# Kernel tuning notes

Hardware: AMD Instinct MI355X
Metric: run time of the kernel (lower is better)

The kernel has to match this reference:

```python
import jax, jax.numpy as jnp
import numpy as np

B, NX, NY = 16, 1024, 1024
DIN_X, DIN_Y = 768, 283
DK, DV, NH = 80, 80, 8
HK, HV = DK // NH, DV // NH  # 10, 10
NORM = 1.0 / np.sqrt(HK)


def setup_inputs() -> dict:
    key = jax.random.key(0)
    kx, ky, kq, kk, kv = jax.random.split(key, 5)
    x = jax.random.normal(kx, (B, NX, DIN_X), dtype=jnp.float32)
    y = jax.random.normal(ky, (B, NY, DIN_Y), dtype=jnp.float32)
    attn_mask = jnp.zeros((B, NX, NY), dtype=jnp.float32)  # unused in forward (dead arg in original)
    # torch nn.Linear weights are [out, in]; kaiming-uniform-ish init scale
    Wq = jax.random.normal(kq, (DK, DIN_X), dtype=jnp.float32) / np.sqrt(DIN_X)
    Wk = jax.random.normal(kk, (DK, DIN_Y), dtype=jnp.float32) / np.sqrt(DIN_Y)
    Wv = jax.random.normal(kv, (DV, DIN_Y), dtype=jnp.float32) / np.sqrt(DIN_Y)
    return {"x": x, "y": y, "attn_mask": attn_mask, "Wq": Wq, "Wk": Wk, "Wv": Wv}


def reference(x, y, attn_mask, Wq, Wk, Wv):
    b, n_x, _ = x.shape
    n_y = y.shape[1]
    # projections (Linear, no bias): [B,N,D] @ W^T
    q = (x @ Wq.T).reshape(b, n_x, NH, HK).transpose(0, 2, 1, 3)  # [B,H,Nx,hk]
    k = (y @ Wk.T).reshape(b, n_y, NH, HK).transpose(0, 2, 1, 3)  # [B,H,Ny,hk]
    v = (y @ Wv.T).reshape(b, n_y, NH, HV).transpose(0, 2, 1, 3)  # [B,H,Ny,hv]
    scores = jnp.einsum("bhqd,bhkd->bhqk", q, k) * NORM          # [B,H,Nx,Ny]
    dist = jax.nn.softmax(scores, axis=-1)
    # dropout p=0.5 is identity in eval mode
    att = jnp.einsum("bhqk,bhkd->bhqd", dist, v)                  # [B,H,Nx,hv]
    att = att.transpose(0, 2, 1, 3).reshape(b, n_x, DV)           # [B,Nx,dim_v]
    return att, dist
```

## Files before the change

### kernel.cpp

```cpp
#include <hip/hip_runtime.h>
#include <hip/hip_bf16.h>

#define BB 16
#define NXX 1024
#define NYY 1024
#define DINX 768
#define DINY 283
#define NHH 8
#define HKK 10
#define DKV 80
#define NORMF 0.31622776601683794f

#define QT 32
#define KC 128
#define SLD 1040

__global__ __launch_bounds__(256) void proj_q_kernel(
    const float* __restrict__ X, const float* __restrict__ W, float* __restrict__ Out) {
  const int LDP = 68;
  __shared__ float Xs[32 * 68];
  __shared__ float Ws[80 * 68];
  const int t = threadIdx.x;
  const int rb = blockIdx.x * 32;
  const int tc = t & 15;
  const int tr = t >> 4;

  float acc[2][5];
#pragma unroll
  for (int i = 0; i < 2; ++i)
#pragma unroll
    for (int j = 0; j < 5; ++j) acc[i][j] = 0.f;

  for (int ch = 0; ch < 12; ++ch) {
    const int dk = ch << 6;
    __syncthreads();
#pragma unroll
    for (int i = 0; i < 8; ++i) {
      int idx = i * 256 + t;
      int r = idx >> 6, c = idx & 63;
      Xs[r * LDP + c] = X[(size_t)(rb + r) * DINX + dk + c];
    }
#pragma unroll
    for (int i = 0; i < 20; ++i) {
      int idx = i * 256 + t;
      int r = idx >> 6, c = idx & 63;
      Ws[r * LDP + c] = W[(size_t)r * DINX + dk + c];
    }
    __syncthreads();
#pragma unroll
    for (int dv = 0; dv < 16; ++dv) {
      float4 xv[2], wv[5];
#pragma unroll
      for (int i = 0; i < 2; ++i)
        xv[i] = *(const float4*)&Xs[(tr * 2 + i) * LDP + dv * 4];
#pragma unroll
      for (int j = 0; j < 5; ++j)
        wv[j] = *(const float4*)&Ws[(tc + 16 * j) * LDP + dv * 4];
#pragma unroll
      for (int i = 0; i < 2; ++i)
#pragma unroll
        for (int j = 0; j < 5; ++j) {
          acc[i][j] += xv[i].x * wv[j].x;
          acc[i][j] += xv[i].y * wv[j].y;
          acc[i][j] += xv[i].z * wv[j].z;
          acc[i][j] += xv[i].w * wv[j].w;
        }
    }
  }
#pragma unroll
  for (int i = 0; i < 2; ++i)
#pragma unroll
    for (int j = 0; j < 5; ++j)
      Out[(size_t)(rb + tr * 2 + i) * DKV + tc + 16 * j] = acc[i][j];
}

__global__ __launch_bounds__(256) void proj_kv_kernel(
    const float* __restrict__ Y, const float* __restrict__ WK, const float* __restrict__ WV,
    float* __restrict__ OutK, float* __restrict__ OutV) {
  const int LDP = 36;
  __shared__ float Xs[32 * 36];
  __shared__ float Ws[160 * 36];
  const int t = threadIdx.x;
  const int rb = blockIdx.x * 32;
  const int tc = t & 15;
  const int tr = t >> 4;

  float acc[2][10];
#pragma unroll
  for (int i = 0; i < 2; ++i)
#pragma unroll
    for (int j = 0; j < 10; ++j) acc[i][j] = 0.f;

  for (int ch = 0; ch < 9; ++ch) {
    const int dk = ch << 5;
    __syncthreads();
#pragma unroll
    for (int i = 0; i < 4; ++i) {
      int idx = i * 256 + t;
      int r = idx >> 5, c = idx & 31;
      int d = dk + c;
      Xs[r * LDP + c] = (d < DINY) ? Y[(size_t)(rb + r) * DINY + d] : 0.f;
    }
#pragma unroll
    for (int i = 0; i < 20; ++i) {
      int idx = i * 256 + t;
      int r = idx >> 5, c = idx & 31;
      int d = dk + c;
      float v = 0.f;
      if (d < DINY) v = (r < 80) ? WK[(size_t)r * DINY + d] : WV[(size_t)(r - 80) * DINY + d];
      Ws[r * LDP + c] = v;
    }
    __syncthreads();
#pragma unroll
    for (int dv = 0; dv < 8; ++dv) {
      float4 xv[2], wv[10];
#pragma unroll
      for (int i = 0; i < 2; ++i)
        xv[i] = *(const float4*)&Xs[(tr * 2 + i) * LDP + dv * 4];
#pragma unroll
      for (int j = 0; j < 5; ++j) {
        wv[j] = *(const float4*)&Ws[(tc + 16 * j) * LDP + dv * 4];
        wv[5 + j] = *(const float4*)&Ws[(80 + tc + 16 * j) * LDP + dv * 4];
      }
#pragma unroll
      for (int i = 0; i < 2; ++i)
#pragma unroll
        for (int j = 0; j < 10; ++j) {
          acc[i][j] += xv[i].x * wv[j].x;
          acc[i][j] += xv[i].y * wv[j].y;
          acc[i][j] += xv[i].z * wv[j].z;
          acc[i][j] += xv[i].w * wv[j].w;
        }
    }
  }
#pragma unroll
  for (int i = 0; i < 2; ++i)
#pragma unroll
    for (int j = 0; j < 5; ++j) {
      OutK[(size_t)(rb + tr * 2 + i) * DKV + tc + 16 * j] = acc[i][j];
      OutV[(size_t)(rb + tr * 2 + i) * DKV + tc + 16 * j] = acc[i][5 + j];
    }
}

__global__ __launch_bounds__(512) void attn_kernel(
    const float* __restrict__ Qw, const float* __restrict__ Kw,
    const float* __restrict__ Vw, float* __restrict__ out_att,
    float* __restrict__ out_dist) {
  __shared__ __hip_bfloat16 S[QT * SLD];
  __shared__ float Ks[KC * 12];
  __shared__ float Vs[KC * 12];
  __shared__ float rls[QT];

  const int t = threadIdx.x;
  const int bid = blockIdx.x;
  const int qt = bid & 31;
  const int h = (bid >> 5) & 7;
  const int b = bid >> 8;

  const int q = t >> 4;
  const int kl = t & 15;
  const int qg = qt * QT + q;

  float qr[10];
  {
    const float2* qp = (const float2*)(Qw + ((size_t)b * NXX + qg) * DKV + h * HKK);
#pragma unroll
    for (int dd = 0; dd < 5; ++dd) {
      float2 v = qp[dd];
      qr[2 * dd] = v.x * NORMF;
      qr[2 * dd + 1] = v.y * NORMF;
    }
  }

  float acc[10];
#pragma unroll
  for (int d = 0; d < 10; ++d) acc[d] = 0.f;
  float lsum = 0.f;

  for (int ch = 0; ch < NYY / KC; ++ch) {
    __syncthreads();
    if (t < 2 * KC) {
      const int r = t & (KC - 1);
      const float2* src = (const float2*)(((t < KC) ? Kw : Vw) +
          ((size_t)b * NYY + ch * KC + r) * DKV + h * HKK);
      float2* dst = (float2*)(((t < KC) ? Ks : Vs) + r * 12);
#pragma unroll
      for (int dd = 0; dd < 5; ++dd) dst[dd] = src[dd];
    }
    __syncthreads();
#pragma unroll
    for (int j = 0; j < KC / 16; ++j) {
      const int k = (j << 4) + kl;
      const float* kp = &Ks[k * 12];
      float4 k0 = *(const float4*)kp;
      float4 k1 = *(const float4*)(kp + 4);
      float2 k2 = *(const float2*)(kp + 8);
      float s = qr[0] * k0.x + qr[1] * k0.y + qr[2] * k0.z + qr[3] * k0.w +
                qr[4] * k1.x + qr[5] * k1.y + qr[6] * k1.z + qr[7] * k1.w +
                qr[8] * k2.x + qr[9] * k2.y;
      float p = __expf(s);
      lsum += p;
      const float* vp = &Vs[k * 12];
      float4 v0 = *(const float4*)vp;
      float4 v1 = *(const float4*)(vp + 4);
      float2 v2 = *(const float2*)(vp + 8);
      acc[0] += p * v0.x; acc[1] += p * v0.y; acc[2] += p * v0.z; acc[3] += p * v0.w;
      acc[4] += p * v1.x; acc[5] += p * v1.y; acc[6] += p * v1.z; acc[7] += p * v1.w;
      acc[8] += p * v2.x; acc[9] += p * v2.y;
      S[q * SLD + (ch << 7) + k] = __float2bfloat16(p);
    }
  }

#pragma unroll
  for (int o = 8; o; o >>= 1) {
    lsum += __shfl_xor(lsum, o);
#pragma unroll
    for (int d = 0; d < 10; ++d) acc[d] += __shfl_xor(acc[d], o);
  }
  const float rl = 1.0f / lsum;

  if (kl == 0) {
    rls[q] = rl;
    float2* ap = (float2*)(out_att + ((size_t)b * NXX + qg) * DKV + h * HKK);
#pragma unroll
    for (int dd = 0; dd < 5; ++dd)
      ap[dd] = make_float2(acc[2 * dd] * rl, acc[2 * dd + 1] * rl);
  }
  __syncthreads();

  const size_t dbase = (((size_t)(b * NHH + h)) * NXX + qt * QT) * NYY;
#pragma unroll 2
  for (int it = 0; it < 16; ++it) {
    const int e = it * 2048 + t * 4;
    const int qq = e >> 10;
    const int kk = e & 1023;
    uint2 w = *(const uint2*)&S[qq * SLD + kk];
    const float rlq = rls[qq];
    float4 o;
    o.x = __uint_as_float(w.x << 16) * rlq;
    o.y = __uint_as_float(w.x & 0xffff0000u) * rlq;
    o.z = __uint_as_float(w.y << 16) * rlq;
    o.w = __uint_as_float(w.y & 0xffff0000u) * rlq;
    *(float4*)(out_dist + dbase + (size_t)qq * NYY + kk) = o;
  }
}

extern "C" void kernel_launch(void* const* d_in, const int* in_sizes, int n_in,
                              void* d_out, int out_size, void* d_ws, size_t ws_size,
                              hipStream_t stream) {
  (void)in_sizes; (void)n_in; (void)out_size; (void)ws_size;
  const float* x = (const float*)d_in[0];
  const float* y = (const float*)d_in[1];
  const float* Wq = (const float*)d_in[3];
  const float* Wk = (const float*)d_in[4];
  const float* Wv = (const float*)d_in[5];

  float* out = (float*)d_out;
  float* att_out = out;
  float* dist_out = out + (size_t)BB * NXX * DKV;

  float* Qw = (float*)d_ws;
  float* Kw = Qw + (size_t)BB * NXX * DKV;
  float* Vw = Kw + (size_t)BB * NYY * DKV;

  proj_q_kernel<<<NXX * BB / 32, 256, 0, stream>>>(x, Wq, Qw);
  proj_kv_kernel<<<NYY * BB / 32, 256, 0, stream>>>(y, Wk, Wv, Kw, Vw);
  attn_kernel<<<BB * NHH * 32, 512, 0, stream>>>(Qw, Kw, Vw, att_out, dist_out);
}
```

Measured before the change: 463.0 us.

## Register-block four queries per thread in attention and merge projection kernels

After: 1.574 ms. +240.0%, slower.

```diff
diff --git a/kernel.cpp b/kernel.cpp
--- a/kernel.cpp
+++ b/kernel.cpp
@@ -15,134 +15,108 @@
 #define KC 128
 #define SLD 1040
 
-__global__ __launch_bounds__(256) void proj_q_kernel(
-    const float* __restrict__ X, const float* __restrict__ W, float* __restrict__ Out) {
-  const int LDP = 68;
-  __shared__ float Xs[32 * 68];
-  __shared__ float Ws[80 * 68];
+__global__ __launch_bounds__(512, 4) void proj_kernel(
+    const float* __restrict__ X, const float* __restrict__ Y,
+    const float* __restrict__ Wq, const float* __restrict__ Wk, const float* __restrict__ Wv,
+    float* __restrict__ Qw, float* __restrict__ Kw, float* __restrict__ Vw) {
+  __shared__ float Xs[64 * 68];
+  __shared__ float Ws[160 * 68];
   const int t = threadIdx.x;
-  const int rb = blockIdx.x * 32;
+  const bool isQ = (blockIdx.x < 256);
+  const int rb = (isQ ? blockIdx.x : blockIdx.x - 256) * 64;
   const int tc = t & 15;
   const int tr = t >> 4;
 
-  float acc[2][5];
-#pragma unroll
-  for (int i = 0; i < 2; ++i)
-#pragma unroll
-    for (int j = 0; j < 5; ++j) acc[i][j] = 0.f;
-
-  for (int ch = 0; ch < 12; ++ch) {
-    const int dk = ch << 6;
-    __syncthreads();
-#pragma unroll
-    for (int i = 0; i < 8; ++i) {
-      int idx = i * 256 + t;
-      int r = idx >> 6, c = idx & 63;
-      Xs[r * LDP + c] = X[(size_t)(rb + r) * DINX + dk + c];
-    }
-#pragma unroll
-    for (int i = 0; i < 20; ++i) {
-      int idx = i * 256 + t;
-      int r = idx >> 6, c = idx & 63;
-      Ws[r * LDP + c] = W[(size_t)r * DINX + dk + c];
-    }
-    __syncthreads();
-#pragma unroll
-    for (int dv = 0; dv < 16; ++dv) {
-      float4 xv[2], wv[5];
-#pragma unroll
-      for (int i = 0; i < 2; ++i)
-        xv[i] = *(const float4*)&Xs[(tr * 2 + i) * LDP + dv * 4];
+  if (isQ) {
+    float acc[2][5];
+#pragma unroll
+    for (int i = 0; i < 2; ++i)
+#pragma unroll
+      for (int j = 0; j < 5; ++j) acc[i][j] = 0.f;
+
+    for (int ch = 0; ch < 12; ++ch) {
+      const int dk = ch << 6;
+      __syncthreads();
+      for (int u = t; u < 1024; u += 512) {
+        int r = u >> 4, c4 = u & 15;
+        *(float4*)&Xs[r * 68 + c4 * 4] = *(const float4*)&X[(size_t)(rb + r) * DINX + dk + c4 * 4];
+      }
+      for (int u = t; u < 1280; u += 512) {
+        int r = u >> 4, c4 = u & 15;
+        *(float4*)&Ws[r * 68 + c4 * 4] = *(const float4*)&Wq[(size_t)r * DINX + dk + c4 * 4];
+      }
+      __syncthreads();
+#pragma unroll
+      for (int dv = 0; dv < 16; ++dv) {
+        float4 xv0 = *(const float4*)&Xs[(tr * 2 + 0) * 68 + dv * 4];
+        float4 xv1 = *(const float4*)&Xs[(tr * 2 + 1) * 68 + dv * 4];
+        float4 wv[5];
+#pragma unroll
+        for (int j = 0; j < 5; ++j)
+          wv[j] = *(const float4*)&Ws[(tc + 16 * j) * 68 + dv * 4];
+#pragma unroll
+        for (int j = 0; j < 5; ++j) {
+          acc[0][j] += xv0.x * wv[j].x + xv0.y * wv[j].y + xv0.z * wv[j].z + xv0.w * wv[j].w;
+          acc[1][j] += xv1.x * wv[j].x + xv1.y * wv[j].y + xv1.z * wv[j].z + xv1.w * wv[j].w;
+        }
+      }
+    }
+#pragma unroll
+    for (int i = 0; i < 2; ++i)
 #pragma unroll
       for (int j = 0; j < 5; ++j)
-        wv[j] = *(const float4*)&Ws[(tc + 16 * j) * LDP + dv * 4];
-#pragma unroll
-      for (int i = 0; i < 2; ++i)
+        Qw[(size_t)(rb + tr * 2 + i) * DKV + tc + 16 * j] = acc[i][j];
+  } else {
+    float acc[2][10];
+#pragma unroll
+    for (int i = 0; i < 2; ++i)
+#pragma unroll
+      for (int j = 0; j < 10; ++j) acc[i][j] = 0.f;
+
+    for (int ch = 0; ch < 5; ++ch) {
+      const int dk = ch << 6;
+      __syncthreads();
+      for (int u = t; u < 4096; u += 512) {
+        int r = u >> 6, c = u & 63;
+        int d = dk + c;
+        Xs[r * 68 + c] = (d < DINY) ? Y[(size_t)(rb + r) * DINY + d] : 0.f;
+      }
+      for (int u = t; u < 10240; u += 512) {
+        int r = u >> 6, c = u & 63;
+        int d = dk + c;
+        float v = 0.f;
+        if (d < DINY) v = (r < 80) ? Wk[(size_t)r * DINY + d] : Wv[(size_t)(r - 80) * DINY + d];
+        Ws[r * 68 + c] = v;
+      }
+      __syncthreads();
+#pragma unroll
+      for (int dv = 0; dv < 16; ++dv) {
+        float4 xv0 = *(const float4*)&Xs[(tr * 2 + 0) * 68 + dv * 4];
+        float4 xv1 = *(const float4*)&Xs[(tr * 2 + 1) * 68 + dv * 4];
+        float4 wv[10];
 #pragma unroll
         for (int j = 0; j < 5; ++j) {
-          acc[i][j] += xv[i].x * wv[j].x;
-          acc[i][j] += xv[i].y * wv[j].y;
-          acc[i][j] += xv[i].z * wv[j].z;
-          acc[i][j] += xv[i].w * wv[j].w;
+          wv[j] = *(const float4*)&Ws[(tc + 16 * j) * 68 + dv * 4];
+          wv[5 + j] = *(const float4*)&Ws[(80 + tc + 16 * j) * 68 + dv * 4];
         }
-    }
-  }
-#pragma unroll
-  for (int i = 0; i < 2; ++i)
-#pragma unroll
-    for (int j = 0; j < 5; ++j)
-      Out[(size_t)(rb + tr * 2 + i) * DKV + tc + 16 * j] = acc[i][j];
+#pragma unroll
+        for (int j = 0; j < 10; ++j) {
+          acc[0][j] += xv0.x * wv[j].x + xv0.y * wv[j].y + xv0.z * wv[j].z + xv0.w * wv[j].w;
+          acc[1][j] += xv1.x * wv[j].x + xv1.y * wv[j].y + xv1.z * wv[j].z + xv1.w * wv[j].w;
+        }
+      }
+    }
+#pragma unroll
+    for (int i = 0; i < 2; ++i)
+#pragma unroll
+      for (int j = 0; j < 5; ++j) {
+        Kw[(size_t)(rb + tr * 2 + i) * DKV + tc + 16 * j] = acc[i][j];
+        Vw[(size_t)(rb + tr * 2 + i) * DKV + tc + 16 * j] = acc[i][5 + j];
+      }
+  }
 }
 
-__global__ __launch_bounds__(256) void proj_kv_kernel(
-    const float* __restrict__ Y, const float* __restrict__ WK, const float* __restrict__ WV,
-    float* __restrict__ OutK, float* __restrict__ OutV) {
-  const int LDP = 36;
-  __shared__ float Xs[32 * 36];
-  __shared__ float Ws[160 * 36];
-  const int t = threadIdx.x;
-  const int rb = blockIdx.x * 32;
-  const int tc = t & 15;
-  const int tr = t >> 4;
-
-  float acc[2][10];
-#pragma unroll
-  for (int i = 0; i < 2; ++i)
-#pragma unroll
-    for (int j = 0; j < 10; ++j) acc[i][j] = 0.f;
-
-  for (int ch = 0; ch < 9; ++ch) {
-    const int dk = ch << 5;
-    __syncthreads();
-#pragma unroll
-    for (int i = 0; i < 4; ++i) {
-      int idx = i * 256 + t;
-      int r = idx >> 5, c = idx & 31;
-      int d = dk + c;
-      Xs[r * LDP + c] = (d < DINY) ? Y[(size_t)(rb + r) * DINY + d] : 0.f;
-    }
-#pragma unroll
-    for (int i = 0; i < 20; ++i) {
-      int idx = i * 256 + t;
-      int r = idx >> 5, c = idx & 31;
-      int d = dk + c;
-      float v = 0.f;
-      if (d < DINY) v = (r < 80) ? WK[(size_t)r * DINY + d] : WV[(size_t)(r - 80) * DINY + d];
-      Ws[r * LDP + c] = v;
-    }
-    __syncthreads();
-#pragma unroll
-    for (int dv = 0; dv < 8; ++dv) {
-      float4 xv[2], wv[10];
-#pragma unroll
-      for (int i = 0; i < 2; ++i)
-        xv[i] = *(const float4*)&Xs[(tr * 2 + i) * LDP + dv * 4];
-#pragma unroll
-      for (int j = 0; j < 5; ++j) {
-        wv[j] = *(const float4*)&Ws[(tc + 16 * j) * LDP + dv * 4];
-        wv[5 + j] = *(const float4*)&Ws[(80 + tc + 16 * j) * LDP + dv * 4];
-      }
-#pragma unroll
-      for (int i = 0; i < 2; ++i)
-#pragma unroll
-        for (int j = 0; j < 10; ++j) {
-          acc[i][j] += xv[i].x * wv[j].x;
-          acc[i][j] += xv[i].y * wv[j].y;
-          acc[i][j] += xv[i].z * wv[j].z;
-          acc[i][j] += xv[i].w * wv[j].w;
-        }
-    }
-  }
-#pragma unroll
-  for (int i = 0; i < 2; ++i)
-#pragma unroll
-    for (int j = 0; j < 5; ++j) {
-      OutK[(size_t)(rb + tr * 2 + i) * DKV + tc + 16 * j] = acc[i][j];
-      OutV[(size_t)(rb + tr * 2 + i) * DKV + tc + 16 * j] = acc[i][5 + j];
-    }
-}
-
-__global__ __launch_bounds__(512) void attn_kernel(
+__global__ __launch_bounds__(512, 4) void attn_kernel(
     const float* __restrict__ Qw, const float* __restrict__ Kw,
     const float* __restrict__ Vw, float* __restrict__ out_att,
     float* __restrict__ out_dist) {
@@ -157,90 +131,108 @@
   const int h = (bid >> 5) & 7;
   const int b = bid >> 8;
 
-  const int q = t >> 4;
-  const int kl = t & 15;
-  const int qg = qt * QT + q;
-
-  float qr[10];
-  {
-    const float2* qp = (const float2*)(Qw + ((size_t)b * NXX + qg) * DKV + h * HKK);
+  const int w = t >> 6;
+  const int kl = t & 63;
+
+  float qr[4][10];
+#pragma unroll
+  for (int qi = 0; qi < 4; ++qi) {
+    const float2* qp = (const float2*)(Qw + ((size_t)b * NXX + qt * QT + w * 4 + qi) * DKV + h * HKK);
 #pragma unroll
     for (int dd = 0; dd < 5; ++dd) {
       float2 v = qp[dd];
-      qr[2 * dd] = v.x * NORMF;
-      qr[2 * dd + 1] = v.y * NORMF;
-    }
-  }
-
-  float acc[10];
-#pragma unroll
-  for (int d = 0; d < 10; ++d) acc[d] = 0.f;
-  float lsum = 0.f;
+      qr[qi][2 * dd] = v.x * NORMF;
+      qr[qi][2 * dd + 1] = v.y * NORMF;
+    }
+  }
+
+  float acc[4][10];
+#pragma unroll
+  for (int qi = 0; qi < 4; ++qi)
+#pragma unroll
+    for (int d = 0; d < 10; ++d) acc[qi][d] = 0.f;
+  float lsum[4] = {0.f, 0.f, 0.f, 0.f};
 
   for (int ch = 0; ch < NYY / KC; ++ch) {
     __syncthreads();
-    if (t < 2 * KC) {
-      const int r = t & (KC - 1);
-      const float2* src = (const float2*)(((t < KC) ? Kw : Vw) +
-          ((size_t)b * NYY + ch * KC + r) * DKV + h * HKK);
-      float2* dst = (float2*)(((t < KC) ? Ks : Vs) + r * 12);
-#pragma unroll
-      for (int dd = 0; dd < 5; ++dd) dst[dd] = src[dd];
+    for (int u = t; u < 1280; u += 512) {
+      int m = (u >= 640);
+      int i = m ? u - 640 : u;
+      int row = i / 5, j = i - row * 5;
+      const float* src = (m ? Vw : Kw) + ((size_t)b * NYY + ch * KC + row) * DKV + h * HKK + j * 2;
+      float2 v = *(const float2*)src;
+      *(float2*)((m ? Vs : Ks) + row * 12 + j * 2) = v;
     }
     __syncthreads();
 #pragma unroll
-    for (int j = 0; j < KC / 16; ++j) {
-      const int k = (j << 4) + kl;
+    for (int kk = 0; kk < 2; ++kk) {
+      const int k = (kk << 6) + kl;
       const float* kp = &Ks[k * 12];
       float4 k0 = *(const float4*)kp;
       float4 k1 = *(const float4*)(kp + 4);
       float2 k2 = *(const float2*)(kp + 8);
-      float s = qr[0] * k0.x + qr[1] * k0.y + qr[2] * k0.z + qr[3] * k0.w +
-                qr[4] * k1.x + qr[5] * k1.y + qr[6] * k1.z + qr[7] * k1.w +
-                qr[8] * k2.x + qr[9] * k2.y;
-      float p = __expf(s);
-      lsum += p;
+      float p[4];
+#pragma unroll
+      for (int qi = 0; qi < 4; ++qi) {
+        float s = qr[qi][0] * k0.x + qr[qi][1] * k0.y + qr[qi][2] * k0.z + qr[qi][3] * k0.w +
+                  qr[qi][4] * k1.x + qr[qi][5] * k1.y + qr[qi][6] * k1.z + qr[qi][7] * k1.w +
+                  qr[qi][8] * k2.x + qr[qi][9] * k2.y;
+        p[qi] = __expf(s);
+        lsum[qi] += p[qi];
+        S[(w * 4 + qi) * SLD + (ch << 7) + k] = __float2bfloat16(p[qi]);
+      }
       const float* vp = &Vs[k * 12];
       float4 v0 = *(const float4*)vp;
       float4 v1 = *(const float4*)(vp + 4);
       float2 v2 = *(const float2*)(vp + 8);
-      acc[0] += p * v0.x; acc[1] += p * v0.y; acc[2] += p * v0.z; acc[3] += p * v0.w;
-      acc[4] += p * v1.x; acc[5] += p * v1.y; acc[6] += p * v1.z; acc[7] += p * v1.w;
-      acc[8] += p * v2.x; acc[9] += p * v2.y;
-      S[q * SLD + (ch << 7) + k] = __float2bfloat16(p);
-    }
-  }
-
-#pragma unroll
-  for (int o = 8; o; o >>= 1) {
-    lsum += __shfl_xor(lsum, o);
-#pragma unroll
-    for (int d = 0; d < 10; ++d) acc[d] += __shfl_xor(acc[d], o);
-  }
-  const float rl = 1.0f / lsum;
+#pragma unroll
+      for (int qi = 0; qi < 4; ++qi) {
+        acc[qi][0] += p[qi] * v0.x; acc[qi][1] += p[qi] * v0.y;
+        acc[qi][2] += p[qi] * v0.z; acc[qi][3] += p[qi] * v0.w;
+        acc[qi][4] += p[qi] * v1.x; acc[qi][5] += p[qi] * v1.y;
+        acc[qi][6] += p[qi] * v1.z; acc[qi][7] += p[qi] * v1.w;
+        acc[qi][8] += p[qi] * v2.x; acc[qi][9] += p[qi] * v2.y;
+      }
+    }
+  }
+
+#pragma unroll
+  for (int off = 32; off; off >>= 1) {
+#pragma unroll
+    for (int qi = 0; qi < 4; ++qi) {
+      lsum[qi] += __shfl_xor(lsum[qi], off);
+#pragma unroll
+      for (int d = 0; d < 10; ++d) acc[qi][d] += __shfl_xor(acc[qi][d], off);
+    }
+  }
 
   if (kl == 0) {
-    rls[q] = rl;
-    float2* ap = (float2*)(out_att + ((size_t)b * NXX + qg) * DKV + h * HKK);
-#pragma unroll
-    for (int dd = 0; dd < 5; ++dd)
-      ap[dd] = make_float2(acc[2 * dd] * rl, acc[2 * dd + 1] * rl);
+#pragma unroll
+    for (int qi = 0; qi < 4; ++qi) {
+      const int q = w * 4 + qi;
+      const float rl = 1.0f / lsum[qi];
+      rls[q] = rl;
+      float* ap = out_att + ((size_t)b * NXX + qt * QT + q) * DKV + h * HKK;
+#pragma unroll
+      for (int dd = 0; dd < 5; ++dd)
+        *(float2*)&ap[2 * dd] = make_float2(acc[qi][2 * dd] * rl, acc[qi][2 * dd + 1] * rl);
+    }
   }
   __syncthreads();
 
   const size_t dbase = (((size_t)(b * NHH + h)) * NXX + qt * QT) * NYY;
 #pragma unroll 2
   for (int it = 0; it < 16; ++it) {
-    const int e = it * 2048 + t * 4;
+    const int e = it * 2048 + (t << 2);
     const int qq = e >> 10;
     const int kk = e & 1023;
-    uint2 w = *(const uint2*)&S[qq * SLD + kk];
+    uint2 wv = *(const uint2*)&S[qq * SLD + kk];
     const float rlq = rls[qq];
     float4 o;
-    o.x = __uint_as_float(w.x << 16) * rlq;
-    o.y = __uint_as_float(w.x & 0xffff0000u) * rlq;
-    o.z = __uint_as_float(w.y << 16) * rlq;
-    o.w = __uint_as_float(w.y & 0xffff0000u) * rlq;
+    o.x = __uint_as_float(wv.x << 16) * rlq;
+    o.y = __uint_as_float(wv.x & 0xffff0000u) * rlq;
+    o.z = __uint_as_float(wv.y << 16) * rlq;
+    o.w = __uint_as_float(wv.y & 0xffff0000u) * rlq;
     *(float4*)(out_dist + dbase + (size_t)qq * NYY + kk) = o;
   }
 }
@@ -263,7 +255,6 @@
   float* Kw = Qw + (size_t)BB * NXX * DKV;
   float* Vw = Kw + (size_t)BB * NYY * DKV;
 
-  proj_q_kernel<<<NXX * BB / 32, 256, 0, stream>>>(x, Wq, Qw);
-  proj_kv_kernel<<<NYY * BB / 32, 256, 0, stream>>>(y, Wk, Wv, Kw, Vw);
+  proj_kernel<<<512, 512, 0, stream>>>(x, y, Wq, Wk, Wv, Qw, Kw, Vw);
   attn_kernel<<<BB * NHH * 32, 512, 0, stream>>>(Qw, Kw, Vw, att_out, dist_out);
 }
```
